# Optimization experiments

Hardware: AMD Instinct MI355X
Metric: run time of the kernel (lower is better)

The kernel has to match this reference:

```python
import jax, jax.numpy as jnp
import numpy as np

NU, NI, D, H, E, NQ = 200000, 100000, 64, 64, 1000000, 100000


def setup_inputs() -> dict:
    key = jax.random.key(0)
    ks = jax.random.split(key, 16)
    s = 0.05
    inp = {
        'user_emb': jax.random.normal(ks[0], (NU, D), jnp.float32) * s,
        'item_emb': jax.random.normal(ks[1], (NI, D), jnp.float32) * s,
        'W1': jax.random.normal(ks[2], (6, D, H), jnp.float32) * s,
        'b1': jnp.zeros((6, H), jnp.float32),
        'W2': jax.random.normal(ks[3], (6, H, H), jnp.float32) * s,
        'b2': jnp.zeros((6, H), jnp.float32),
        'dec_w1': jax.random.normal(ks[4], (2 * H, H), jnp.float32) * s,
        'dec_b1': jnp.zeros((H,), jnp.float32),
        'dec_w2': jax.random.normal(ks[5], (H, 4), jnp.float32) * s,
        'dec_b2': jnp.zeros((4,), jnp.float32),
    }
    for name, k in [('edge_view', ks[6]), ('edge_save', ks[7]), ('edge_buy', ks[8])]:
        src = jax.random.randint(k, (E,), 0, NU, jnp.int64 if jax.config.jax_enable_x64 else jnp.int32)
        dst = jax.random.randint(jax.random.fold_in(k, 1), (E,), 0, NI, src.dtype)
        inp[name] = jnp.stack([src, dst])  # [2, E], row0=user, row1=item
    inp['user_ids'] = jax.random.randint(ks[9], (NQ,), 0, NU, jnp.int32)
    inp['item_ids'] = jax.random.randint(ks[10], (NQ,), 0, NI, jnp.int32)
    return inp


def _gcn_conv(h_src, src, dst, n_src, n_dst, W, b):
    # GCNConv (add_self_loops=False) on a bipartite relation:
    # out[d] = sum_e 1/sqrt(deg_src[src_e]) * 1/sqrt(deg_dst[d]) * (x W)[src_e] + b
    h = h_src @ W  # [n_src, H]
    ones = jnp.ones(src.shape[0], h.dtype)
    deg_s = jax.ops.segment_sum(ones, src, num_segments=n_src)
    deg_d = jax.ops.segment_sum(ones, dst, num_segments=n_dst)
    inv_s = jnp.where(deg_s > 0, jax.lax.rsqrt(jnp.maximum(deg_s, 1.0)), 0.0)
    inv_d = jnp.where(deg_d > 0, jax.lax.rsqrt(jnp.maximum(deg_d, 1.0)), 0.0)
    norm = inv_s[src] * inv_d[dst]  # [E]
    msg = h[src] * norm[:, None]    # [E, H]  (dominant memory traffic)
    return jax.ops.segment_sum(msg, dst, num_segments=n_dst) + b


def _hetero_layer(xu, xi, edges, W, b, aggr):
    # relations 0..2: user->item (view,save,buy); 3..5: item->user (reverses)
    item_outs = jnp.stack([_gcn_conv(xu, e[0], e[1], NU, NI, W[k], b[k])
                           for k, e in enumerate(edges)])
    user_outs = jnp.stack([_gcn_conv(xi, e[1], e[0], NI, NU, W[k + 3], b[k + 3])
                           for k, e in enumerate(edges)])
    if aggr == 'max':
        return user_outs.max(0), item_outs.max(0)
    return user_outs.sum(0), item_outs.sum(0)


def reference(user_emb, item_emb, W1, b1, W2, b2, dec_w1, dec_b1, dec_w2, dec_b2,
              edge_view, edge_save, edge_buy, user_ids, item_ids):
    edges = [edge_view, edge_save, edge_buy]
    xu, xi = _hetero_layer(user_emb, item_emb, edges, W1, b1, 'max')
    xu, xi = jax.nn.relu(xu), jax.nn.relu(xi)
    xu, xi = _hetero_layer(xu, xi, edges, W2, b2, 'sum')
    edge_emb = jnp.concatenate([xu[user_ids], xi[item_ids]], axis=-1)  # [NQ, 2H]
    h = jax.nn.relu(edge_emb @ dec_w1 + dec_b1)  # dropout in eval mode = identity
    return h @ dec_w2 + dec_b2  # [NQ, 4]
```

## Files before the change

### kernel.cpp

```cpp
#include <hip/hip_runtime.h>
#include <hip/hip_fp16.h>
#include <math.h>

#define NUV 200000
#define NIV 100000
#define EV  1000000
#define NQV 100000
#define NC  (3 * NIV + 3 * NUV)

struct alignas(8) H4 { __half2 a, b; };

__global__ __launch_bounds__(256) void k_tohalf(const float* __restrict__ in,
                                                __half* __restrict__ out, int n4) {
    int i = blockIdx.x * 256 + threadIdx.x;
    if (i < n4) {
        float4 v = ((const float4*)in)[i];
        H4 o;
        o.a = __floats2half2_rn(v.x, v.y);
        o.b = __floats2half2_rn(v.z, v.w);
        ((H4*)out)[i] = o;
    }
}

__global__ __launch_bounds__(256) void k_count(const int* __restrict__ e0,
                                               const int* __restrict__ e1,
                                               const int* __restrict__ e2,
                                               int* __restrict__ cnt,
                                               int* __restrict__ rk_i,
                                               int* __restrict__ rk_u) {
    int k = blockIdx.y;
    const int* ed = (k == 0) ? e0 : (k == 1) ? e1 : e2;
    int e = blockIdx.x * 256 + threadIdx.x;
    if (e < EV) {
        int u = ed[e], i = ed[EV + e];
        rk_i[(size_t)k * EV + e] = atomicAdd(&cnt[k * NIV + i], 1);
        rk_u[(size_t)k * EV + e] = atomicAdd(&cnt[3 * NIV + k * NUV + u], 1);
    }
}

__global__ __launch_bounds__(256) void k_invf(const int* __restrict__ cnt,
                                              float* __restrict__ invs) {
    int i = blockIdx.x * 256 + threadIdx.x;
    if (i < NC) {
        int c = cnt[i];
        invs[i] = (c > 0) ? (1.0f / sqrtf((float)c)) : 0.0f;
    }
}

__global__ __launch_bounds__(256) void k_scan1(const int* __restrict__ cnt,
                                               int* __restrict__ S,
                                               int* __restrict__ bsum) {
    __shared__ int tmp[256];
    int idx = blockIdx.x * 256 + threadIdx.x;
    int v = (idx < NC) ? cnt[idx] : 0;
    tmp[threadIdx.x] = v;
    __syncthreads();
    for (int off = 1; off < 256; off <<= 1) {
        int t = (threadIdx.x >= off) ? tmp[threadIdx.x - off] : 0;
        __syncthreads();
        tmp[threadIdx.x] += t;
        __syncthreads();
    }
    if (idx < NC) S[idx] = tmp[threadIdx.x] - v;
    if (threadIdx.x == 255) bsum[blockIdx.x] = tmp[255];
}

__global__ __launch_bounds__(64) void k_scan2(int* __restrict__ bsum, int nb) {
    int lane = threadIdx.x;
    int carry = 0;
    for (int base = 0; base < nb; base += 64) {
        int i = base + lane;
        int v = (i < nb) ? bsum[i] : 0;
        int orig = v;
        #pragma unroll
        for (int off = 1; off < 64; off <<= 1) {
            int t = __shfl_up(v, off, 64);
            if (lane >= off) v += t;
        }
        if (i < nb) bsum[i] = carry + v - orig;
        carry += __shfl(v, 63, 64);
    }
}

__global__ __launch_bounds__(256) void k_scan3(int* __restrict__ S,
                                               const int* __restrict__ bsum) {
    int idx = blockIdx.x * 256 + threadIdx.x;
    if (idx < NC) S[idx] += bsum[blockIdx.x];
    if (idx == 0) S[NC] = 6 * EV;
}

__global__ __launch_bounds__(256) void k_fill(const int* __restrict__ e0,
                                              const int* __restrict__ e1,
                                              const int* __restrict__ e2,
                                              const float* __restrict__ invs,
                                              const int* __restrict__ S,
                                              const int* __restrict__ rk_i,
                                              const int* __restrict__ rk_u,
                                              float2* __restrict__ ent) {
    int k = blockIdx.y;
    const int* ed = (k == 0) ? e0 : (k == 1) ? e1 : e2;
    int e = blockIdx.x * 256 + threadIdx.x;
    if (e < EV) {
        int u = ed[e], i = ed[EV + e];
        float nm = invs[k * NIV + i] * invs[3 * NIV + k * NUV + u];
        int p1 = S[k * NIV + i] + rk_i[(size_t)k * EV + e];
        ent[p1] = make_float2(__int_as_float(u), nm);
        int p2 = S[3 * NIV + k * NUV + u] + rk_u[(size_t)k * EV + e];
        ent[p2] = make_float2(__int_as_float(i), nm);
    }
}

template <int MODE, bool HOUT>
__global__ __launch_bounds__(256, 4) void k_agg(const __half* __restrict__ x_i,
                                                const __half* __restrict__ x_u,
                                                const float2* __restrict__ ent,
                                                const int* __restrict__ S,
                                                const float* __restrict__ Wall,
                                                const float* __restrict__ ball,
                                                void* __restrict__ out_i,
                                                void* __restrict__ out_u) {
    __shared__ float sW[4096];
    __shared__ float sAcc[16 * 68];
    const int nb_i = NIV / 16;
    bool item_side = blockIdx.x < nb_i;
    const __half* x = item_side ? x_i : x_u;
    const float* Wb = item_side ? Wall : Wall + 3 * 4096;
    const float* bb = item_side ? ball : ball + 192;
    void* outp      = item_side ? out_i : out_u;
    int n_dst       = item_side ? NIV : NUV;
    int seg_base    = item_side ? 0 : 3 * NIV;
    int d0          = (item_side ? blockIdx.x : (blockIdx.x - nb_i)) * 16;

    int wave = threadIdx.x >> 6;
    int lane = threadIdx.x & 63;
    int eg   = lane >> 3;
    int fh   = lane & 7;
    int r2 = threadIdx.x >> 4;
    int g  = threadIdx.x & 15;

    float4 res = make_float4(0.f, 0.f, 0.f, 0.f);
    for (int k = 0; k < 3; k++) {
        __syncthreads();
        int idx = seg_base + k * n_dst + d0 + wave * 4;
        int v0 = S[idx], v1 = S[idx + 1], v2 = S[idx + 2], v3 = S[idx + 3], v4 = S[idx + 4];
        {
            const float4* wsrc = (const float4*)(Wb + (size_t)k * 4096);
            float4* wdst = (float4*)sW;
            #pragma unroll
            for (int i = 0; i < 4; i++) wdst[threadIdx.x + 256 * i] = wsrc[threadIdx.x + 256 * i];
        }
        {
            int st[4] = {v0, v1, v2, v3};
            int en[4] = {v1, v2, v3, v4};
            int maxlen = max(max(v1 - v0, v2 - v1), max(v3 - v2, v4 - v3));
            int maxit = (maxlen + 7) >> 3;
            float af[4][8];
            #pragma unroll
            for (int n = 0; n < 4; n++)
                #pragma unroll
                for (int j = 0; j < 8; j++) af[n][j] = 0.f;
            for (int it = 0; it < maxit; it++) {
                #pragma unroll
                for (int n = 0; n < 4; n++) {
                    int p = st[n] + (it << 3) + eg;
                    if (p < en[n]) {
                        float2 e = ent[p];
                        int s = __float_as_int(e.x);
                        float4 raw = *(const float4*)(x + (size_t)s * 64 + fh * 8);
                        const __half2* h2 = (const __half2*)&raw;
                        #pragma unroll
                        for (int j = 0; j < 4; j++) {
                            float2 f = __half22float2(h2[j]);
                            af[n][2 * j]     = fmaf(f.x, e.y, af[n][2 * j]);
                            af[n][2 * j + 1] = fmaf(f.y, e.y, af[n][2 * j + 1]);
                        }
                    }
                }
            }
            #pragma unroll
            for (int n = 0; n < 4; n++) {
                #pragma unroll
                for (int j = 0; j < 8; j++) {
                    af[n][j] += __shfl_xor(af[n][j], 8, 64);
                    af[n][j] += __shfl_xor(af[n][j], 16, 64);
                    af[n][j] += __shfl_xor(af[n][j], 32, 64);
                }
                if (lane < 8) {
                    int row = wave * 4 + n;
                    *(float4*)&sAcc[row * 68 + lane * 8] =
                        make_float4(af[n][0], af[n][1], af[n][2], af[n][3]);
                    *(float4*)&sAcc[row * 68 + lane * 8 + 4] =
                        make_float4(af[n][4], af[n][5], af[n][6], af[n][7]);
                }
            }
        }
        __syncthreads();
        float4 y = *(const float4*)&bb[k * 64 + g * 4];
        #pragma unroll
        for (int c = 0; c < 64; c++) {
            float a = sAcc[r2 * 68 + c];
            float4 w = *(const float4*)&sW[c * 64 + g * 4];
            y.x = fmaf(a, w.x, y.x);
            y.y = fmaf(a, w.y, y.y);
            y.z = fmaf(a, w.z, y.z);
            y.w = fmaf(a, w.w, y.w);
        }
        if (k == 0) {
            res = y;
        } else if (MODE == 0) {
            res.x = fmaxf(res.x, y.x); res.y = fmaxf(res.y, y.y);
            res.z = fmaxf(res.z, y.z); res.w = fmaxf(res.w, y.w);
        } else {
            res.x += y.x; res.y += y.y; res.z += y.z; res.w += y.w;
        }
    }
    if (MODE == 0) {
        res.x = fmaxf(res.x, 0.f); res.y = fmaxf(res.y, 0.f);
        res.z = fmaxf(res.z, 0.f); res.w = fmaxf(res.w, 0.f);
    }
    if (HOUT) {
        H4 o;
        o.a = __floats2half2_rn(res.x, res.y);
        o.b = __floats2half2_rn(res.z, res.w);
        *(H4*)((__half*)outp + (size_t)(d0 + r2) * 64 + g * 4) = o;
    } else {
        *(float4*)((float*)outp + (size_t)(d0 + r2) * 64 + g * 4) = res;
    }
}

__global__ __launch_bounds__(256) void k_decoder(const float* __restrict__ xu,
                                                 const float* __restrict__ xi,
                                                 const int* __restrict__ uids,
                                                 const int* __restrict__ iids,
                                                 const float* __restrict__ w1,
                                                 const float* __restrict__ b1,
                                                 const float* __restrict__ w2,
                                                 const float* __restrict__ b2,
                                                 float* __restrict__ out) {
    __shared__ float sW1[128 * 64];
    __shared__ float sE[16 * 132];
    __shared__ float sH[16 * 68];
    __shared__ float sW2[64 * 4];
    {
        const float4* wsrc = (const float4*)w1;
        float4* wdst = (float4*)sW1;
        #pragma unroll
        for (int i = 0; i < 8; i++) wdst[threadIdx.x + 256 * i] = wsrc[threadIdx.x + 256 * i];
        if (threadIdx.x < 64) {
            float4 v = ((const float4*)w2)[threadIdx.x];
            ((float4*)sW2)[threadIdx.x] = v;
        }
    }
    int q0 = blockIdx.x * 16;
    {
        int q = threadIdx.x >> 4;
        int p = threadIdx.x & 15;
        int uid = uids[q0 + q];
        int iid = iids[q0 + q];
        float4 vu = *(const float4*)&xu[(size_t)uid * 64 + p * 4];
        float4 vi = *(const float4*)&xi[(size_t)iid * 64 + p * 4];
        *(float4*)&sE[q * 132 + p * 4] = vu;
        *(float4*)&sE[q * 132 + 64 + p * 4] = vi;
    }
    __syncthreads();
    {
        int r = threadIdx.x >> 4;
        int g = threadIdx.x & 15;
        float4 y = *(const float4*)&b1[g * 4];
        #pragma unroll
        for (int c = 0; c < 128; c++) {
            float a = sE[r * 132 + c];
            float4 w = *(const float4*)&sW1[c * 64 + g * 4];
            y.x = fmaf(a, w.x, y.x);
            y.y = fmaf(a, w.y, y.y);
            y.z = fmaf(a, w.z, y.z);
            y.w = fmaf(a, w.w, y.w);
        }
        y.x = fmaxf(y.x, 0.f); y.y = fmaxf(y.y, 0.f);
        y.z = fmaxf(y.z, 0.f); y.w = fmaxf(y.w, 0.f);
        *(float4*)&sH[r * 68 + g * 4] = y;
    }
    __syncthreads();
    if (threadIdx.x < 64) {
        int q = threadIdx.x >> 2;
        int oc = threadIdx.x & 3;
        float acc = b2[oc];
        #pragma unroll
        for (int c = 0; c < 64; c++)
            acc = fmaf(sH[q * 68 + c], sW2[c * 4 + oc], acc);
        out[(size_t)(q0 + q) * 4 + oc] = acc;
    }
}

extern "C" void kernel_launch(void* const* d_in, const int* in_sizes, int n_in,
                              void* d_out, int out_size, void* d_ws, size_t ws_size,
                              hipStream_t stream) {
    const float* user_emb = (const float*)d_in[0];
    const float* item_emb = (const float*)d_in[1];
    const float* W1 = (const float*)d_in[2];
    const float* b1 = (const float*)d_in[3];
    const float* W2 = (const float*)d_in[4];
    const float* b2 = (const float*)d_in[5];
    const float* dw1 = (const float*)d_in[6];
    const float* db1 = (const float*)d_in[7];
    const float* dw2 = (const float*)d_in[8];
    const float* db2 = (const float*)d_in[9];
    const int* e0 = (const int*)d_in[10];
    const int* e1 = (const int*)d_in[11];
    const int* e2 = (const int*)d_in[12];
    const int* uids = (const int*)d_in[13];
    const int* iids = (const int*)d_in[14];
    float* out = (float*)d_out;
    (void)in_sizes; (void)n_in; (void)out_size; (void)ws_size;

    char* base = (char*)d_ws;
    size_t off = 0;
    int*    cnt  = (int*)(base + off);    off += (size_t)NC * 4;
    int*    S    = (int*)(base + off);    off += (size_t)(NC + 8) * 4;
    int*    bsum = (int*)(base + off);    off += (size_t)4096 * 4;
    float*  invs = (float*)(base + off);  off += (size_t)NC * 4;
    int*    rki  = (int*)(base + off);    off += (size_t)3 * EV * 4;
    int*    rku  = (int*)(base + off);    off += (size_t)3 * EV * 4;
    float2* ent  = (float2*)(base + off); off += (size_t)6 * EV * 8;
    __half* he_u = (__half*)(base + off); off += (size_t)NUV * 64 * 2;
    __half* he_i = (__half*)(base + off); off += (size_t)NIV * 64 * 2;
    __half* xu1h = (__half*)(base + off); off += (size_t)NUV * 64 * 2;
    __half* xi1h = (__half*)(base + off); off += (size_t)NIV * 64 * 2;
    float*  xu2  = (float*)(base + off);  off += (size_t)NUV * 64 * 4;
    float*  xi2  = (float*)(base + off);  off += (size_t)NIV * 64 * 4;

    const int EB  = (EV + 255) / 256;
    const int SB1 = (NC + 255) / 256;
    const int AGGB = NIV / 16 + NUV / 16;

    k_tohalf<<<(NUV * 64 / 4 + 255) / 256, 256, 0, stream>>>(user_emb, he_u, NUV * 64 / 4);
    k_tohalf<<<(NIV * 64 / 4 + 255) / 256, 256, 0, stream>>>(item_emb, he_i, NIV * 64 / 4);

    hipMemsetAsync(cnt, 0, (size_t)NC * 4, stream);
    k_count<<<dim3(EB, 3), 256, 0, stream>>>(e0, e1, e2, cnt, rki, rku);
    k_invf<<<SB1, 256, 0, stream>>>(cnt, invs);
    k_scan1<<<SB1, 256, 0, stream>>>(cnt, S, bsum);
    k_scan2<<<1, 64, 0, stream>>>(bsum, SB1);
    k_scan3<<<SB1, 256, 0, stream>>>(S, bsum);
    k_fill<<<dim3(EB, 3), 256, 0, stream>>>(e0, e1, e2, invs, S, rki, rku, ent);

    k_agg<0, true><<<AGGB, 256, 0, stream>>>(he_u, he_i, ent, S, W1, b1, xi1h, xu1h);
    k_agg<1, false><<<AGGB, 256, 0, stream>>>(xu1h, xi1h, ent, S, W2, b2, xi2, xu2);

    k_decoder<<<NQV / 16, 256, 0, stream>>>(xu2, xi2, uids, iids,
                                            dw1, db1, dw2, db2, out);
}
```

Measured before the change: 1.444 ms.

## Gather all three relations in one loop with more loads in flight

The aggregation kernel now walks all three relations' CSR segments in a single loop. Each lane loads a 4-half slice (16 lanes per row, 4 edges per step), and all 12 entry loads are issued before the 12 feature gathers, with clamping and a zero weight standing in for branches. This raises memory-level parallelism and drops the per-relation barriers and the shared-memory staging of W, which is now read from global/cache. Separately, the two fp16 conversions become one launch and the inverse-sqrt kernel is folded into the first scan pass to cut launches. The costs are more registers (acc[3][4][4], ev, raw), which may lower occupancy, and wasted work when the three relations have uneven segment lengths.

Measured after the change: 1.651 ms. 1.14x slower.

```diff
diff --git a/kernel.cpp b/kernel.cpp
--- a/kernel.cpp
+++ b/kernel.cpp
@@ -7,18 +7,26 @@
 #define EV  1000000
 #define NQV 100000
 #define NC  (3 * NIV + 3 * NUV)
+#define EV6 (6 * EV)
 
 struct alignas(8) H4 { __half2 a, b; };
 
-__global__ __launch_bounds__(256) void k_tohalf(const float* __restrict__ in,
-                                                __half* __restrict__ out, int n4) {
+__global__ __launch_bounds__(256) void k_tohalf(const float* __restrict__ inu,
+                                                const float* __restrict__ ini,
+                                                __half* __restrict__ outu,
+                                                __half* __restrict__ outi) {
+    const int NU4 = NUV * 16;
+    const int NTOT = NU4 + NIV * 16;
     int i = blockIdx.x * 256 + threadIdx.x;
-    if (i < n4) {
-        float4 v = ((const float4*)in)[i];
+    if (i < NTOT) {
+        const float* in = (i < NU4) ? inu : ini;
+        __half* out = (i < NU4) ? outu : outi;
+        int j = (i < NU4) ? i : (i - NU4);
+        float4 v = ((const float4*)in)[j];
         H4 o;
         o.a = __floats2half2_rn(v.x, v.y);
         o.b = __floats2half2_rn(v.z, v.w);
-        ((H4*)out)[i] = o;
+        ((H4*)out)[j] = o;
     }
 }
 
@@ -38,21 +46,14 @@
     }
 }
 
-__global__ __launch_bounds__(256) void k_invf(const int* __restrict__ cnt,
-                                              float* __restrict__ invs) {
-    int i = blockIdx.x * 256 + threadIdx.x;
-    if (i < NC) {
-        int c = cnt[i];
-        invs[i] = (c > 0) ? (1.0f / sqrtf((float)c)) : 0.0f;
-    }
-}
-
 __global__ __launch_bounds__(256) void k_scan1(const int* __restrict__ cnt,
                                                int* __restrict__ S,
-                                               int* __restrict__ bsum) {
+                                               int* __restrict__ bsum,
+                                               float* __restrict__ invs) {
     __shared__ int tmp[256];
     int idx = blockIdx.x * 256 + threadIdx.x;
     int v = (idx < NC) ? cnt[idx] : 0;
+    if (idx < NC) invs[idx] = (v > 0) ? (1.0f / sqrtf((float)v)) : 0.0f;
     tmp[threadIdx.x] = v;
     __syncthreads();
     for (int off = 1; off < 256; off <<= 1) {
@@ -86,7 +87,7 @@
                                                const int* __restrict__ bsum) {
     int idx = blockIdx.x * 256 + threadIdx.x;
     if (idx < NC) S[idx] += bsum[blockIdx.x];
-    if (idx == 0) S[NC] = 6 * EV;
+    if (idx == 0) S[NC] = EV6;
 }
 
 __global__ __launch_bounds__(256) void k_fill(const int* __restrict__ e0,
@@ -119,8 +120,7 @@
                                                 const float* __restrict__ ball,
                                                 void* __restrict__ out_i,
                                                 void* __restrict__ out_u) {
-    __shared__ float sW[4096];
-    __shared__ float sAcc[16 * 68];
+    __shared__ float sAcc[3][16 * 68];
     const int nb_i = NIV / 16;
     bool item_side = blockIdx.x < nb_i;
     const __half* x = item_side ? x_i : x_u;
@@ -133,73 +133,92 @@
 
     int wave = threadIdx.x >> 6;
     int lane = threadIdx.x & 63;
-    int eg   = lane >> 3;
-    int fh   = lane & 7;
+    int eg   = lane >> 4;
+    int fq   = lane & 15;
     int r2 = threadIdx.x >> 4;
     int g  = threadIdx.x & 15;
 
+    int sb[3][5];
+    #pragma unroll
+    for (int k = 0; k < 3; k++) {
+        int idx = seg_base + k * n_dst + d0 + wave * 4;
+        #pragma unroll
+        for (int j = 0; j < 5; j++) sb[k][j] = S[idx + j];
+    }
+    int mx = 0;
+    #pragma unroll
+    for (int k = 0; k < 3; k++)
+        #pragma unroll
+        for (int n = 0; n < 4; n++) mx = max(mx, sb[k][n + 1] - sb[k][n]);
+    int maxit = (mx + 3) >> 2;
+
+    float acc[3][4][4];
+    #pragma unroll
+    for (int k = 0; k < 3; k++)
+        #pragma unroll
+        for (int n = 0; n < 4; n++)
+            #pragma unroll
+            for (int j = 0; j < 4; j++) acc[k][n][j] = 0.f;
+
+    for (int it = 0; it < maxit; it++) {
+        int base = (it << 2) + eg;
+        float2 ev[3][4];
+        #pragma unroll
+        for (int k = 0; k < 3; k++)
+            #pragma unroll
+            for (int n = 0; n < 4; n++) {
+                int p = sb[k][n] + base;
+                int pc = min(p, EV6 - 1);
+                ev[k][n] = ent[pc];
+            }
+        float2 raw[3][4];
+        float nm[3][4];
+        #pragma unroll
+        for (int k = 0; k < 3; k++)
+            #pragma unroll
+            for (int n = 0; n < 4; n++) {
+                int p = sb[k][n] + base;
+                nm[k][n] = (p < sb[k][n + 1]) ? ev[k][n].y : 0.f;
+                int s = __float_as_int(ev[k][n].x);
+                raw[k][n] = *(const float2*)(x + (size_t)s * 64 + fq * 4);
+            }
+        #pragma unroll
+        for (int k = 0; k < 3; k++)
+            #pragma unroll
+            for (int n = 0; n < 4; n++) {
+                const __half2* h2 = (const __half2*)&raw[k][n];
+                float2 f0 = __half22float2(h2[0]);
+                float2 f1 = __half22float2(h2[1]);
+                acc[k][n][0] = fmaf(f0.x, nm[k][n], acc[k][n][0]);
+                acc[k][n][1] = fmaf(f0.y, nm[k][n], acc[k][n][1]);
+                acc[k][n][2] = fmaf(f1.x, nm[k][n], acc[k][n][2]);
+                acc[k][n][3] = fmaf(f1.y, nm[k][n], acc[k][n][3]);
+            }
+    }
+    #pragma unroll
+    for (int k = 0; k < 3; k++)
+        #pragma unroll
+        for (int n = 0; n < 4; n++) {
+            #pragma unroll
+            for (int j = 0; j < 4; j++) {
+                acc[k][n][j] += __shfl_xor(acc[k][n][j], 16, 64);
+                acc[k][n][j] += __shfl_xor(acc[k][n][j], 32, 64);
+            }
+            if (lane < 16)
+                *(float4*)&sAcc[k][(wave * 4 + n) * 68 + fq * 4] =
+                    make_float4(acc[k][n][0], acc[k][n][1], acc[k][n][2], acc[k][n][3]);
+        }
+    __syncthreads();
+
     float4 res = make_float4(0.f, 0.f, 0.f, 0.f);
+    #pragma unroll
     for (int k = 0; k < 3; k++) {
-        __syncthreads();
-        int idx = seg_base + k * n_dst + d0 + wave * 4;
-        int v0 = S[idx], v1 = S[idx + 1], v2 = S[idx + 2], v3 = S[idx + 3], v4 = S[idx + 4];
-        {
-            const float4* wsrc = (const float4*)(Wb + (size_t)k * 4096);
-            float4* wdst = (float4*)sW;
-            #pragma unroll
-            for (int i = 0; i < 4; i++) wdst[threadIdx.x + 256 * i] = wsrc[threadIdx.x + 256 * i];
-        }
-        {
-            int st[4] = {v0, v1, v2, v3};
-            int en[4] = {v1, v2, v3, v4};
-            int maxlen = max(max(v1 - v0, v2 - v1), max(v3 - v2, v4 - v3));
-            int maxit = (maxlen + 7) >> 3;
-            float af[4][8];
-            #pragma unroll
-            for (int n = 0; n < 4; n++)
-                #pragma unroll
-                for (int j = 0; j < 8; j++) af[n][j] = 0.f;
-            for (int it = 0; it < maxit; it++) {
-                #pragma unroll
-                for (int n = 0; n < 4; n++) {
-                    int p = st[n] + (it << 3) + eg;
-                    if (p < en[n]) {
-                        float2 e = ent[p];
-                        int s = __float_as_int(e.x);
-                        float4 raw = *(const float4*)(x + (size_t)s * 64 + fh * 8);
-                        const __half2* h2 = (const __half2*)&raw;
-                        #pragma unroll
-                        for (int j = 0; j < 4; j++) {
-                            float2 f = __half22float2(h2[j]);
-                            af[n][2 * j]     = fmaf(f.x, e.y, af[n][2 * j]);
-                            af[n][2 * j + 1] = fmaf(f.y, e.y, af[n][2 * j + 1]);
-                        }
-                    }
-                }
-            }
-            #pragma unroll
-            for (int n = 0; n < 4; n++) {
-                #pragma unroll
-                for (int j = 0; j < 8; j++) {
-                    af[n][j] += __shfl_xor(af[n][j], 8, 64);
-                    af[n][j] += __shfl_xor(af[n][j], 16, 64);
-                    af[n][j] += __shfl_xor(af[n][j], 32, 64);
-                }
-                if (lane < 8) {
-                    int row = wave * 4 + n;
-                    *(float4*)&sAcc[row * 68 + lane * 8] =
-                        make_float4(af[n][0], af[n][1], af[n][2], af[n][3]);
-                    *(float4*)&sAcc[row * 68 + lane * 8 + 4] =
-                        make_float4(af[n][4], af[n][5], af[n][6], af[n][7]);
-                }
-            }
-        }
-        __syncthreads();
+        const float* Wk = Wb + (size_t)k * 4096;
         float4 y = *(const float4*)&bb[k * 64 + g * 4];
         #pragma unroll
         for (int c = 0; c < 64; c++) {
-            float a = sAcc[r2 * 68 + c];
-            float4 w = *(const float4*)&sW[c * 64 + g * 4];
+            float a = sAcc[k][r2 * 68 + c];
+            float4 w = *(const float4*)&Wk[c * 64 + g * 4];
             y.x = fmaf(a, w.x, y.x);
             y.y = fmaf(a, w.y, y.y);
             y.z = fmaf(a, w.z, y.z);
@@ -321,7 +340,7 @@
     float*  invs = (float*)(base + off);  off += (size_t)NC * 4;
     int*    rki  = (int*)(base + off);    off += (size_t)3 * EV * 4;
     int*    rku  = (int*)(base + off);    off += (size_t)3 * EV * 4;
-    float2* ent  = (float2*)(base + off); off += (size_t)6 * EV * 8;
+    float2* ent  = (float2*)(base + off); off += (size_t)EV6 * 8;
     __half* he_u = (__half*)(base + off); off += (size_t)NUV * 64 * 2;
     __half* he_i = (__half*)(base + off); off += (size_t)NIV * 64 * 2;
     __half* xu1h = (__half*)(base + off); off += (size_t)NUV * 64 * 2;
@@ -332,14 +351,13 @@
     const int EB  = (EV + 255) / 256;
     const int SB1 = (NC + 255) / 256;
     const int AGGB = NIV / 16 + NUV / 16;
-
-    k_tohalf<<<(NUV * 64 / 4 + 255) / 256, 256, 0, stream>>>(user_emb, he_u, NUV * 64 / 4);
-    k_tohalf<<<(NIV * 64 / 4 + 255) / 256, 256, 0, stream>>>(item_emb, he_i, NIV * 64 / 4);
+    const int THB = ((NUV + NIV) * 16 + 255) / 256;
+
+    k_tohalf<<<THB, 256, 0, stream>>>(user_emb, item_emb, he_u, he_i);
 
     hipMemsetAsync(cnt, 0, (size_t)NC * 4, stream);
     k_count<<<dim3(EB, 3), 256, 0, stream>>>(e0, e1, e2, cnt, rki, rku);
-    k_invf<<<SB1, 256, 0, stream>>>(cnt, invs);
-    k_scan1<<<SB1, 256, 0, stream>>>(cnt, S, bsum);
+    k_scan1<<<SB1, 256, 0, stream>>>(cnt, S, bsum, invs);
     k_scan2<<<1, 64, 0, stream>>>(bsum, SB1);
     k_scan3<<<SB1, 256, 0, stream>>>(S, bsum);
     k_fill<<<dim3(EB, 3), 256, 0, stream>>>(e0, e1, e2, invs, S, rki, rku, ent);
```
